# Kernel optimization log

Measured on AMD Instinct MI355X. Metric: run time of the kernel, lower is better.

Reference implementation:

```python
import jax, jax.numpy as jnp
import numpy as np

BETA = 0.9
TH = 1.0
SLOPE = 25.0  # fast-sigmoid surrogate slope (spike_grad_slope)

@jax.custom_vjp
def spike_fn(m):
    # Heaviside on (mem - threshold)
    return (m > 0).astype(m.dtype)

def _spike_fwd(m):
    return spike_fn(m), m

def _spike_bwd(m, g):
    # fast-sigmoid surrogate gradient: 1 / (slope*|m| + 1)^2
    return (g / (SLOPE * jnp.abs(m) + 1.0) ** 2,)

spike_fn.defvjp(_spike_fwd, _spike_bwd)


def setup_inputs() -> dict:
    key = jax.random.key(0)
    k1, k2, k3 = jax.random.split(key, 3)
    T, B, I, H, O = 128, 8192, 2, 256, 2
    x = jax.random.normal(k1, (T, B, I), dtype=jnp.float32)
    # xavier_uniform with gain=1: limit = sqrt(6/(fan_in+fan_out))
    lim1 = float(np.sqrt(6.0 / (I + H)))
    lim2 = float(np.sqrt(6.0 / (H + O)))
    W1 = jax.random.uniform(k2, (H, I), jnp.float32, -lim1, lim1)
    W2 = jax.random.uniform(k3, (O, H), jnp.float32, -lim2, lim2)
    return {"x": x, "W1": W1, "W2": W2}


def reference(x, W1, W2):
    # Precompute all per-step input currents in one GEMM: [T,B,H]
    cur = jnp.einsum('tbi,hi->tbh', x, W1)
    B, H = cur.shape[1], cur.shape[2]
    mem0 = jnp.zeros((B, H), cur.dtype)

    def step(mem, c):
        # snntorch Leaky (reset_mechanism='subtract'):
        # reset based on PREVIOUS mem's spike, then leaky integrate, then fire
        reset = spike_fn(mem - TH)
        mem_new = BETA * mem + c - reset * TH
        spk = spike_fn(mem_new - TH)
        # original code detaches mem between steps (1-step truncated BPTT)
        return jax.lax.stop_gradient(mem_new), spk

    _, spk_rec = jax.lax.scan(step, mem0, cur)  # spk_rec: [T,B,H]
    spk_avg = spk_rec[-10:].mean(0)             # [B,H]
    out = jnp.einsum('bh,oh->bo', spk_avg, W2)  # [B,O]
    return out
```

## Files before the change

### kernel.cpp

```cpp
#include <hip/hip_runtime.h>


#define T_STEPS 128
#define BATCH   8192
#define HID     256
#define TAIL    10
#define RH      8
#define LB      64
#define NWAVE   4
#define HG      8
#define NBG     (BATCH / LB)
#define PF      8

__global__ __launch_bounds__(256) void snn_scan(const float* __restrict__ x,
                                                const float* __restrict__ W1,
                                                const float* __restrict__ W2,
                                                float2* __restrict__ partial) {
    const int tid   = threadIdx.x;
    const int lane  = tid & 63;
    const int wave  = tid >> 6;
    const int bg    = blockIdx.x & (NBG - 1);
    const int hg    = blockIdx.x >> 7;
    const int b     = bg * LB + lane;
    const int hbase = hg * (NWAVE * RH) + wave * RH;

    float w0[RH], w1[RH];
#pragma unroll
    for (int r = 0; r < RH; ++r) {
        w0[r] = W1[2 * (hbase + r)];
        w1[r] = W1[2 * (hbase + r) + 1];
    }

    const float2* xb = (const float2*)x + b;

    float mem[RH], spk[RH], cnt[RH];
#pragma unroll
    for (int r = 0; r < RH; ++r) { mem[r] = 0.0f; spk[r] = 0.0f; cnt[r] = 0.0f; }

#define STEP(r, xa, xc)                                                           \
    {                                                                             \
        const float c = __fadd_rn(__fmul_rn((xa), w0[r]), __fmul_rn((xc), w1[r]));\
        mem[r] = __fsub_rn(__fadd_rn(__fmul_rn(0.9f, mem[r]), c), spk[r]);        \
        spk[r] = (mem[r] > 1.0f) ? 1.0f : 0.0f;                                   \
    }

    float2 buf[PF];
#pragma unroll
    for (int j = 0; j < PF; ++j) buf[j] = xb[(size_t)j * BATCH];

    for (int tb = 0; tb < T_STEPS - 2 * PF; tb += PF) {
#pragma unroll
        for (int j = 0; j < PF; ++j) {
            const float2 xv = buf[j];
            buf[j] = xb[(size_t)(tb + PF + j) * BATCH];
#pragma unroll
            for (int r = 0; r < RH; ++r) STEP(r, xv.x, xv.y)
        }
    }

    float2 buf2[PF];
#pragma unroll
    for (int j = 0; j < PF; ++j) buf2[j] = xb[(size_t)(T_STEPS - PF + j) * BATCH];

#pragma unroll
    for (int j = 0; j < PF; ++j) {
        const float2 xv = buf[j];
#pragma unroll
        for (int r = 0; r < RH; ++r) {
            STEP(r, xv.x, xv.y)
            if (j >= PF - 2) cnt[r] += spk[r];
        }
    }
#pragma unroll
    for (int j = 0; j < PF; ++j) {
        const float2 xv = buf2[j];
#pragma unroll
        for (int r = 0; r < RH; ++r) {
            STEP(r, xv.x, xv.y)
            cnt[r] += spk[r];
        }
    }
#undef STEP

    float p0 = 0.0f, p1 = 0.0f;
#pragma unroll
    for (int r = 0; r < RH; ++r) {
        const float avg = cnt[r] / 10.0f;
        p0 = __fadd_rn(p0, __fmul_rn(avg, W2[hbase + r]));
        p1 = __fadd_rn(p1, __fmul_rn(avg, W2[HID + hbase + r]));
    }

    __shared__ float2 red[NWAVE][LB];
    red[wave][lane] = make_float2(p0, p1);
    __syncthreads();
    if (wave == 0) {
        const float2 a0 = red[0][lane], a1 = red[1][lane];
        const float2 a2 = red[2][lane], a3 = red[3][lane];
        float2 s;
        s.x = __fadd_rn(__fadd_rn(a0.x, a1.x), __fadd_rn(a2.x, a3.x));
        s.y = __fadd_rn(__fadd_rn(a0.y, a1.y), __fadd_rn(a2.y, a3.y));
        partial[(size_t)hg * BATCH + b] = s;
    }
}

__global__ __launch_bounds__(256) void snn_reduce(const float2* __restrict__ partial,
                                                  float2* __restrict__ out) {
    const int b = blockIdx.x * 256 + threadIdx.x;
    float sx = 0.0f, sy = 0.0f;
#pragma unroll
    for (int hg = 0; hg < HG; ++hg) {
        const float2 p = partial[(size_t)hg * BATCH + b];
        sx = __fadd_rn(sx, p.x);
        sy = __fadd_rn(sy, p.y);
    }
    out[b] = make_float2(sx, sy);
}

extern "C" void kernel_launch(void* const* d_in, const int* in_sizes, int n_in,
                              void* d_out, int out_size, void* d_ws, size_t ws_size,
                              hipStream_t stream) {
    const float* x  = (const float*)d_in[0];
    const float* W1 = (const float*)d_in[1];
    const float* W2 = (const float*)d_in[2];
    float2* out     = (float2*)d_out;
    float2* partial = (float2*)d_ws;

    snn_scan<<<NBG * HG, 256, 0, stream>>>(x, W1, W2, partial);
    snn_reduce<<<BATCH / 256, 256, 0, stream>>>(partial, out);
}
```

Baseline: 103.1 us.

## Pack neuron state into float2 vectors and halve rows per wave

Rewrites the per-neuron LIF update to operate on pairs of hidden units using two-wide float vectors, so the compiler can emit packed FP32 math (v_pk_mul/v_pk_add), with contraction disabled to keep rounding identical. Rows per wave drop from 8 to 4 and the hidden-group count doubles to 16, doubling the grid and the number of partial outputs reduced in the second kernel. The aim is fewer VALU instructions per step and more waves for latency hiding. In exchange, each x element is loaded by twice as many blocks and the reduction kernel reads more partials.

```diff
diff --git a/kernel.cpp b/kernel.cpp
--- a/kernel.cpp
+++ b/kernel.cpp
@@ -1,14 +1,17 @@
 #include <hip/hip_runtime.h>
 
+
+typedef float v2f __attribute__((ext_vector_type(2)));
 
 #define T_STEPS 128
 #define BATCH   8192
 #define HID     256
 #define TAIL    10
-#define RH      8
+#define RH      4
+#define NP      (RH / 2)
 #define LB      64
 #define NWAVE   4
-#define HG      8
+#define HG      16
 #define NBG     (BATCH / LB)
 #define PF      8
 
@@ -16,6 +19,7 @@
                                                 const float* __restrict__ W1,
                                                 const float* __restrict__ W2,
                                                 float2* __restrict__ partial) {
+#pragma clang fp contract(off)
     const int tid   = threadIdx.x;
     const int lane  = tid & 63;
     const int wave  = tid >> 6;
@@ -24,24 +28,28 @@
     const int b     = bg * LB + lane;
     const int hbase = hg * (NWAVE * RH) + wave * RH;
 
-    float w0[RH], w1[RH];
+    v2f w0p[NP], w1p[NP];
 #pragma unroll
-    for (int r = 0; r < RH; ++r) {
-        w0[r] = W1[2 * (hbase + r)];
-        w1[r] = W1[2 * (hbase + r) + 1];
+    for (int p = 0; p < NP; ++p) {
+        const int h0 = hbase + 2 * p;
+        w0p[p][0] = W1[2 * h0];     w0p[p][1] = W1[2 * (h0 + 1)];
+        w1p[p][0] = W1[2 * h0 + 1]; w1p[p][1] = W1[2 * (h0 + 1) + 1];
     }
 
     const float2* xb = (const float2*)x + b;
 
-    float mem[RH], spk[RH], cnt[RH];
+    v2f memp[NP], spkp[NP], cntp[NP];
 #pragma unroll
-    for (int r = 0; r < RH; ++r) { mem[r] = 0.0f; spk[r] = 0.0f; cnt[r] = 0.0f; }
+    for (int p = 0; p < NP; ++p) { memp[p] = (v2f)0.0f; spkp[p] = (v2f)0.0f; cntp[p] = (v2f)0.0f; }
 
-#define STEP(r, xa, xc)                                                           \
-    {                                                                             \
-        const float c = __fadd_rn(__fmul_rn((xa), w0[r]), __fmul_rn((xc), w1[r]));\
-        mem[r] = __fsub_rn(__fadd_rn(__fmul_rn(0.9f, mem[r]), c), spk[r]);        \
-        spk[r] = (mem[r] > 1.0f) ? 1.0f : 0.0f;                                   \
+    const v2f beta = 0.9f;
+
+#define STEP(p, xav, xcv)                                                        \
+    {                                                                            \
+        const v2f c = ((xav) * w0p[p]) + ((xcv) * w1p[p]);                       \
+        memp[p] = ((beta * memp[p]) + c) - spkp[p];                              \
+        spkp[p][0] = memp[p][0] > 1.0f ? 1.0f : 0.0f;                            \
+        spkp[p][1] = memp[p][1] > 1.0f ? 1.0f : 0.0f;                            \
     }
 
     float2 buf[PF];
@@ -53,8 +61,10 @@
         for (int j = 0; j < PF; ++j) {
             const float2 xv = buf[j];
             buf[j] = xb[(size_t)(tb + PF + j) * BATCH];
+            const v2f xav = {xv.x, xv.x};
+            const v2f xcv = {xv.y, xv.y};
 #pragma unroll
-            for (int r = 0; r < RH; ++r) STEP(r, xv.x, xv.y)
+            for (int p = 0; p < NP; ++p) STEP(p, xav, xcv)
         }
     }
 
@@ -65,19 +75,23 @@
 #pragma unroll
     for (int j = 0; j < PF; ++j) {
         const float2 xv = buf[j];
+        const v2f xav = {xv.x, xv.x};
+        const v2f xcv = {xv.y, xv.y};
 #pragma unroll
-        for (int r = 0; r < RH; ++r) {
-            STEP(r, xv.x, xv.y)
-            if (j >= PF - 2) cnt[r] += spk[r];
+        for (int p = 0; p < NP; ++p) {
+            STEP(p, xav, xcv)
+            if (j >= PF - 2) cntp[p] += spkp[p];
         }
     }
 #pragma unroll
     for (int j = 0; j < PF; ++j) {
         const float2 xv = buf2[j];
+        const v2f xav = {xv.x, xv.x};
+        const v2f xcv = {xv.y, xv.y};
 #pragma unroll
-        for (int r = 0; r < RH; ++r) {
-            STEP(r, xv.x, xv.y)
-            cnt[r] += spk[r];
+        for (int p = 0; p < NP; ++p) {
+            STEP(p, xav, xcv)
+            cntp[p] += spkp[p];
         }
     }
 #undef STEP
@@ -85,7 +99,8 @@
     float p0 = 0.0f, p1 = 0.0f;
 #pragma unroll
     for (int r = 0; r < RH; ++r) {
-        const float avg = cnt[r] / 10.0f;
+        const float cnt = cntp[r >> 1][r & 1];
+        const float avg = cnt / 10.0f;
         p0 = __fadd_rn(p0, __fmul_rn(avg, W2[hbase + r]));
         p1 = __fadd_rn(p1, __fmul_rn(avg, W2[HID + hbase + r]));
     }
```

Measured after the change: 139.6 us. 1.35x slower.
